# Optimization experiments

Hardware: AMD Instinct MI355X
Metric: run time of the kernel (lower is better)

The kernel has to match this reference:

```python
import jax, jax.numpy as jnp
import numpy as np
from jax import lax

S, B, V = 128, 64, 32000
E, H = 32, 16  # embed dim and hidden dim are hardcoded in the module


def setup_inputs() -> dict:
    key = jax.random.key(0)
    k0, k1, k2, k3, k4, k5 = jax.random.split(key, 6)
    input_batch = jax.random.randint(k0, (S, B), 0, V)
    lookup = jax.random.normal(k1, (V, E), dtype=jnp.float32)
    weight_x = jax.random.normal(k2, (E, H), dtype=jnp.float32) * 0.1
    weight_h = jax.random.normal(k3, (H, H), dtype=jnp.float32) * 0.1
    weight_o = jax.random.normal(k4, (H, V), dtype=jnp.float32) * 0.1
    h0 = jax.random.normal(k5, (B, H), dtype=jnp.float32)  # torch.randn init of H
    return {"input_batch": input_batch, "lookup": lookup, "weight_x": weight_x,
            "weight_h": weight_h, "weight_o": weight_o, "h0": h0}


def reference(input_batch, lookup, weight_x, weight_h, weight_o, h0):
    # Embedding gather: [S, B, E]
    X = lookup[input_batch]

    def step(h, x_t):
        # Elman recurrence: h = tanh(x @ Wx + h @ Wh)
        h_new = jnp.tanh(x_t @ weight_x + h @ weight_h)
        # log(softmax(h @ Wo)) over vocab axis
        logp = jax.nn.log_softmax(h_new @ weight_o, axis=-1)
        return h_new, logp

    _, output = lax.scan(step, h0, X)  # output: [S, B, V]
    return output
```

## Files before the change

### kernel.cpp

```cpp
#include <hip/hip_runtime.h>
#include <math.h>

#define SS 128
#define BB 64
#define VV 32000
#define EE 32
#define HH 16
#define NROW (SS*BB)
#define RT 16

__global__ __launch_bounds__(64) void rnn_recurrence(
        const int*   __restrict__ idx,
        const float* __restrict__ lookup,
        const float* __restrict__ Wx,
        const float* __restrict__ Wh,
        const float* __restrict__ h0,
        float*       __restrict__ Hmat) {
    const int b    = blockIdx.x;
    const int lane = threadIdx.x;
    const int j    = lane & (HH - 1);

    float wxj[EE];
    #pragma unroll
    for (int e = 0; e < EE; ++e) wxj[e] = Wx[e * HH + j];
    float whj[HH];
    #pragma unroll
    for (int k = 0; k < HH; ++k) whj[k] = Wh[k * HH + j];

    float hj = h0[b * HH + j];

    for (int t = 0; t < SS; ++t) {
        const int token = idx[t * BB + b];
        const float xv = lookup[token * EE + (lane & (EE - 1))];

        float a0 = 0.f, a1 = 0.f, a2 = 0.f, a3 = 0.f;
        #pragma unroll
        for (int e = 0; e < EE; e += 4) {
            a0 += __shfl(xv, e)     * wxj[e];
            a1 += __shfl(xv, e + 1) * wxj[e + 1];
            a2 += __shfl(xv, e + 2) * wxj[e + 2];
            a3 += __shfl(xv, e + 3) * wxj[e + 3];
        }
        #pragma unroll
        for (int k = 0; k < HH; k += 4) {
            a0 += __shfl(hj, k)     * whj[k];
            a1 += __shfl(hj, k + 1) * whj[k + 1];
            a2 += __shfl(hj, k + 2) * whj[k + 2];
            a3 += __shfl(hj, k + 3) * whj[k + 3];
        }
        hj = tanhf((a0 + a1) + (a2 + a3));
        if (lane < HH) Hmat[(t * BB + b) * HH + j] = hj;
    }
}

__global__ __launch_bounds__(256) void rnn_lse(
        const float* __restrict__ Hmat,
        const float* __restrict__ Wo,
        float*       __restrict__ lse) {
    const int row0 = blockIdx.x * RT;
    const int tid  = threadIdx.x;

    float s[RT];
    #pragma unroll
    for (int r = 0; r < RT; ++r) s[r] = 0.f;

    for (int j = tid; j < VV / 4; j += 256) {
        float4 wc[HH];
        #pragma unroll
        for (int k = 0; k < HH; ++k)
            wc[k] = ((const float4*)(Wo + k * VV))[j];
        #pragma unroll
        for (int r = 0; r < RT; ++r) {
            const float* h = Hmat + (row0 + r) * HH;
            float l0 = 0.f, l1 = 0.f, l2 = 0.f, l3 = 0.f;
            #pragma unroll
            for (int k = 0; k < HH; ++k) {
                const float hk = h[k];
                l0 += hk * wc[k].x; l1 += hk * wc[k].y;
                l2 += hk * wc[k].z; l3 += hk * wc[k].w;
            }
            s[r] += (__expf(l0) + __expf(l1)) + (__expf(l2) + __expf(l3));
        }
    }

    #pragma unroll
    for (int r = 0; r < RT; ++r) {
        float v = s[r];
        #pragma unroll
        for (int off = 32; off >= 1; off >>= 1)
            v += __shfl_down(v, off);
        s[r] = v;
    }
    __shared__ float red[4][RT];
    const int wave = tid >> 6;
    if ((tid & 63) == 0) {
        #pragma unroll
        for (int r = 0; r < RT; ++r) red[wave][r] = s[r];
    }
    __syncthreads();
    if (tid < RT) {
        const float tot = (red[0][tid] + red[1][tid]) + (red[2][tid] + red[3][tid]);
        lse[row0 + tid] = __logf(tot);
    }
}

__global__ __launch_bounds__(256) void rnn_out(
        const float* __restrict__ Hmat,
        const float* __restrict__ Wo,
        const float* __restrict__ lse,
        float*       __restrict__ out) {
    const int row0 = blockIdx.x * RT;
    const int tid  = threadIdx.x;

    for (int j = tid; j < VV / 4; j += 256) {
        float4 wc[HH];
        #pragma unroll
        for (int k = 0; k < HH; ++k)
            wc[k] = ((const float4*)(Wo + k * VV))[j];
        #pragma unroll
        for (int r = 0; r < RT; ++r) {
            const int row = row0 + r;
            const float* h = Hmat + row * HH;
            float l0 = 0.f, l1 = 0.f, l2 = 0.f, l3 = 0.f;
            #pragma unroll
            for (int k = 0; k < HH; ++k) {
                const float hk = h[k];
                l0 += hk * wc[k].x; l1 += hk * wc[k].y;
                l2 += hk * wc[k].z; l3 += hk * wc[k].w;
            }
            const float m = lse[row];
            float4 o = make_float4(l0 - m, l1 - m, l2 - m, l3 - m);
            ((float4*)(out + (size_t)row * VV))[j] = o;
        }
    }
}

extern "C" void kernel_launch(void* const* d_in, const int* in_sizes, int n_in,
                              void* d_out, int out_size, void* d_ws, size_t ws_size,
                              hipStream_t stream) {
    const int*   idx    = (const int*)  d_in[0];
    const float* lookup = (const float*)d_in[1];
    const float* Wx     = (const float*)d_in[2];
    const float* Wh     = (const float*)d_in[3];
    const float* Wo     = (const float*)d_in[4];
    const float* h0     = (const float*)d_in[5];
    float* out = (float*)d_out;

    float* Hmat = (float*)d_ws;
    float* lse  = Hmat + (size_t)NROW * HH;

    rnn_recurrence<<<BB, 64, 0, stream>>>(idx, lookup, Wx, Wh, h0, Hmat);
    rnn_lse<<<NROW / RT, 256, 0, stream>>>(Hmat, Wo, lse);
    rnn_out<<<NROW / RT, 256, 0, stream>>>(Hmat, Wo, lse, out);
}
```

Baseline: 1.428 ms.

## Fuse LSE and output kernels, prefetch embeddings, use nontemporal output stores

Merges the log-sum-exp pass and the output-writing pass into one kernel, so each block keeps its row LSE values in shared memory instead of going through global memory, and one launch is removed. The recurrence kernel now preloads all token indices and prefetches embedding rows two steps ahead to hide gather latency on the serial critical path. Output writes use nontemporal stores to reduce cache pollution from the 1 GB output stream. Each block still computes the logits twice and carries more live registers.

```diff
diff --git a/kernel.cpp b/kernel.cpp
--- a/kernel.cpp
+++ b/kernel.cpp
@@ -9,6 +9,8 @@
 #define NROW (SS*BB)
 #define RT 16
 
+typedef float f32x4 __attribute__((ext_vector_type(4)));
+
 __global__ __launch_bounds__(64) void rnn_recurrence(
         const int*   __restrict__ idx,
         const float* __restrict__ lookup,
@@ -19,6 +21,7 @@
     const int b    = blockIdx.x;
     const int lane = threadIdx.x;
     const int j    = lane & (HH - 1);
+    const int exl  = lane & (EE - 1);
 
     float wxj[EE];
     #pragma unroll
@@ -27,19 +30,31 @@
     #pragma unroll
     for (int k = 0; k < HH; ++k) whj[k] = Wh[k * HH + j];
 
+    const int tokA = idx[lane * BB + b];
+    const int tokB = idx[(lane + 64) * BB + b];
+
     float hj = h0[b * HH + j];
 
+    int tk0 = __shfl(tokA, 0);
+    float xv_c = lookup[tk0 * EE + exl];
+    int tk1 = __shfl(tokA, 1);
+    float xv_n = lookup[tk1 * EE + exl];
+
     for (int t = 0; t < SS; ++t) {
-        const int token = idx[t * BB + b];
-        const float xv = lookup[token * EE + (lane & (EE - 1))];
+        float xv_f = 0.f;
+        if (t + 2 < SS) {
+            const int tf  = t + 2;
+            const int tok = __shfl((tf & 64) ? tokB : tokA, tf & 63);
+            xv_f = lookup[tok * EE + exl];
+        }
 
         float a0 = 0.f, a1 = 0.f, a2 = 0.f, a3 = 0.f;
         #pragma unroll
         for (int e = 0; e < EE; e += 4) {
-            a0 += __shfl(xv, e)     * wxj[e];
-            a1 += __shfl(xv, e + 1) * wxj[e + 1];
-            a2 += __shfl(xv, e + 2) * wxj[e + 2];
-            a3 += __shfl(xv, e + 3) * wxj[e + 3];
+            a0 += __shfl(xv_c, e)     * wxj[e];
+            a1 += __shfl(xv_c, e + 1) * wxj[e + 1];
+            a2 += __shfl(xv_c, e + 2) * wxj[e + 2];
+            a3 += __shfl(xv_c, e + 3) * wxj[e + 3];
         }
         #pragma unroll
         for (int k = 0; k < HH; k += 4) {
@@ -50,13 +65,15 @@
         }
         hj = tanhf((a0 + a1) + (a2 + a3));
         if (lane < HH) Hmat[(t * BB + b) * HH + j] = hj;
+
+        xv_c = xv_n; xv_n = xv_f;
     }
 }
 
-__global__ __launch_bounds__(256) void rnn_lse(
+__global__ __launch_bounds__(256) void rnn_lse_out(
         const float* __restrict__ Hmat,
         const float* __restrict__ Wo,
-        float*       __restrict__ lse) {
+        float*       __restrict__ out) {
     const int row0 = blockIdx.x * RT;
     const int tid  = threadIdx.x;
 
@@ -64,11 +81,11 @@
     #pragma unroll
     for (int r = 0; r < RT; ++r) s[r] = 0.f;
 
-    for (int j = tid; j < VV / 4; j += 256) {
+    for (int jc = tid; jc < VV / 4; jc += 256) {
         float4 wc[HH];
         #pragma unroll
         for (int k = 0; k < HH; ++k)
-            wc[k] = ((const float4*)(Wo + k * VV))[j];
+            wc[k] = ((const float4*)(Wo + k * VV))[jc];
         #pragma unroll
         for (int r = 0; r < RT; ++r) {
             const float* h = Hmat + (row0 + r) * HH;
@@ -92,6 +109,7 @@
         s[r] = v;
     }
     __shared__ float red[4][RT];
+    __shared__ float lse_sh[RT];
     const int wave = tid >> 6;
     if ((tid & 63) == 0) {
         #pragma unroll
@@ -100,23 +118,19 @@
     __syncthreads();
     if (tid < RT) {
         const float tot = (red[0][tid] + red[1][tid]) + (red[2][tid] + red[3][tid]);
-        lse[row0 + tid] = __logf(tot);
+        lse_sh[tid] = __logf(tot);
     }
-}
+    __syncthreads();
 
-__global__ __launch_bounds__(256) void rnn_out(
-        const float* __restrict__ Hmat,
-        const float* __restrict__ Wo,
-        const float* __restrict__ lse,
-        float*       __restrict__ out) {
-    const int row0 = blockIdx.x * RT;
-    const int tid  = threadIdx.x;
+    float mr[RT];
+    #pragma unroll
+    for (int r = 0; r < RT; ++r) mr[r] = lse_sh[r];
 
-    for (int j = tid; j < VV / 4; j += 256) {
+    for (int jc = tid; jc < VV / 4; jc += 256) {
         float4 wc[HH];
         #pragma unroll
         for (int k = 0; k < HH; ++k)
-            wc[k] = ((const float4*)(Wo + k * VV))[j];
+            wc[k] = ((const float4*)(Wo + k * VV))[jc];
         #pragma unroll
         for (int r = 0; r < RT; ++r) {
             const int row = row0 + r;
@@ -128,9 +142,10 @@
                 l0 += hk * wc[k].x; l1 += hk * wc[k].y;
                 l2 += hk * wc[k].z; l3 += hk * wc[k].w;
             }
-            const float m = lse[row];
-            float4 o = make_float4(l0 - m, l1 - m, l2 - m, l3 - m);
-            ((float4*)(out + (size_t)row * VV))[j] = o;
+            const float m = mr[r];
+            f32x4 o;
+            o.x = l0 - m; o.y = l1 - m; o.z = l2 - m; o.w = l3 - m;
+            __builtin_nontemporal_store(o, (f32x4*)(out + (size_t)row * VV) + jc);
         }
     }
 }
@@ -147,9 +162,7 @@
     float* out = (float*)d_out;
 
     float* Hmat = (float*)d_ws;
-    float* lse  = Hmat + (size_t)NROW * HH;
 
     rnn_recurrence<<<BB, 64, 0, stream>>>(idx, lookup, Wx, Wh, h0, Hmat);
-    rnn_lse<<<NROW / RT, 256, 0, stream>>>(Hmat, Wo, lse);
-    rnn_out<<<NROW / RT, 256, 0, stream>>>(Hmat, Wo, lse, out);
+    rnn_lse_out<<<NROW / RT, 256, 0, stream>>>(Hmat, Wo, out);
 }
```

After: 1.291 ms. 9.6% less time.
